# Performance work log

Hardware: AMD Instinct MI355X
Metric: run time of the kernel (lower is better)

## Reference

```python
import jax, jax.numpy as jnp
import numpy as np

NEG_INF = -9e15  # matches -9000000000000000.0 in torch code
ALPHA = 0.2      # LeakyReLU negative slope


def setup_inputs() -> dict:
    key = jax.random.key(0)
    k1, k2, k3, k4 = jax.random.split(key, 4)
    B, N, Fin, Fout = 8, 2048, 256, 256
    h = jax.random.normal(k1, (B, N, Fin), dtype=jnp.float32)
    adj = jax.random.randint(k2, (B, N, N), 0, 2, dtype=jnp.int32)
    W = jax.random.normal(k3, (Fin, Fout), dtype=jnp.float32) * 0.05
    a = jax.random.normal(k4, (2 * Fout, 1), dtype=jnp.float32) * 0.05
    return {"h": h, "adj": adj, "W": W, "a": a}


def reference(h, adj, W, a):
    # h: [B,N,Fin], adj: [B,N,N], W: [Fin,Fout], a: [2*Fout,1]
    Fout = W.shape[1]
    Wh = jnp.matmul(h, W)                       # [B,N,Fout]
    # Decompose concat-based additive score: e_ij = LReLU(a1.Wh_i + a2.Wh_j)
    a1 = a[:Fout, 0]                            # source-node part
    a2 = a[Fout:, 0]                            # target-node part
    s1 = jnp.einsum('bnf,f->bn', Wh, a1)        # [B,N]
    s2 = jnp.einsum('bnf,f->bn', Wh, a2)        # [B,N]
    e = jax.nn.leaky_relu(s1[:, :, None] + s2[:, None, :], negative_slope=ALPHA)  # [B,N,N]
    attn = jnp.where(adj > 0, e, NEG_INF)
    attn = jax.nn.softmax(attn, axis=2)          # masked softmax over neighbors
    # dropout omitted (deterministic eval-mode reference)
    h_prime = jnp.matmul(attn, Wh)               # [B,N,Fout]
    return h_prime
```

## Files before the change

### kernel.cpp

```cpp
#include <hip/hip_runtime.h>
#include <cstdint>

#define ALPHA 0.2f

constexpr int NB = 8;
constexpr int NN = 2048;
constexpr int NF = 256;

typedef __attribute__((ext_vector_type(8))) short bf16x8;
typedef __attribute__((ext_vector_type(4))) float f32x4;

__device__ __forceinline__ float bf2f(unsigned short u) {
    union { unsigned int i; float f; } v;
    v.i = ((unsigned int)u) << 16;
    return v.f;
}
__device__ __forceinline__ unsigned short f2bf(float f) {
    union { float f; unsigned int i; } v;
    v.f = f;
    v.i += 0x7fffu + ((v.i >> 16) & 1);
    return (unsigned short)(v.i >> 16);
}

__global__ __launch_bounds__(256) void k_wt(const float* __restrict__ W,
                                            unsigned short* __restrict__ WT,
                                            float* __restrict__ s1,
                                            float* __restrict__ s2) {
    const int t = threadIdx.x;
    const int gid = blockIdx.x * 256 + t;
    s1[gid] = 0.f;
    s2[gid] = 0.f;
    const int k = blockIdx.x * 4 + (t >> 6);
    const int f0 = (t & 63) * 4;
    const float4 w = *(const float4*)&W[k * NF + f0];
    WT[(f0 + 0) * NF + k] = f2bf(w.x);
    WT[(f0 + 1) * NF + k] = f2bf(w.y);
    WT[(f0 + 2) * NF + k] = f2bf(w.z);
    WT[(f0 + 3) * NF + k] = f2bf(w.w);
}

__global__ __launch_bounds__(256, 4) void k_wh(const float* __restrict__ h,
                                               const unsigned short* __restrict__ WT,
                                               const float* __restrict__ a,
                                               unsigned short* __restrict__ WhT,
                                               float* __restrict__ s1,
                                               float* __restrict__ s2) {
    __shared__ __align__(16) unsigned short As[64][72];
    __shared__ __align__(16) unsigned short Bs[64][72];
    const int tid = threadIdx.x;
    const int lane = tid & 63;
    const int l16 = lane & 15;
    const int quad = lane >> 4;
    const int wave = tid >> 6;
    const int row0 = (blockIdx.x >> 2) * 64;
    const int col0 = (blockIdx.x & 3) * 64;
    const int bb = row0 >> 11;
    const int n0 = row0 & (NN - 1);
    const int mb = (wave & 1) * 32;
    const int nb = (wave >> 1) * 32;

    f32x4 acc[2][2];
#pragma unroll
    for (int mf = 0; mf < 2; ++mf)
#pragma unroll
        for (int nf = 0; nf < 2; ++nf) acc[mf][nf] = (f32x4){0.f, 0.f, 0.f, 0.f};

    for (int k0 = 0; k0 < NF; k0 += 64) {
#pragma unroll
        for (int it = 0; it < 4; ++it) {
            const int q = tid + it * 256;
            const int r = q >> 4;
            const int k4 = (q & 15) * 4;
            const float4 v = *(const float4*)&h[(size_t)(row0 + r) * NF + k0 + k4];
            ushort4 o;
            o.x = f2bf(v.x); o.y = f2bf(v.y); o.z = f2bf(v.z); o.w = f2bf(v.w);
            *(ushort4*)&As[r][k4] = o;
        }
#pragma unroll
        for (int it = 0; it < 2; ++it) {
            const int q = tid + it * 256;
            const int f = q >> 3;
            const int k8 = (q & 7) * 8;
            *(uint4*)&Bs[f][k8] =
                *(const uint4*)&WT[(size_t)(col0 + f) * NF + k0 + k8];
        }
        __syncthreads();
#pragma unroll
        for (int ks = 0; ks < 64; ks += 32) {
            bf16x8 av[2], bv[2];
#pragma unroll
            for (int mf = 0; mf < 2; ++mf)
                av[mf] = *(const bf16x8*)&As[mb + mf * 16 + l16][ks + quad * 8];
#pragma unroll
            for (int nf = 0; nf < 2; ++nf)
                bv[nf] = *(const bf16x8*)&Bs[nb + nf * 16 + l16][ks + quad * 8];
#pragma unroll
            for (int mf = 0; mf < 2; ++mf)
#pragma unroll
                for (int nf = 0; nf < 2; ++nf)
                    acc[mf][nf] = __builtin_amdgcn_mfma_f32_16x16x32_bf16(
                        av[mf], bv[nf], acc[mf][nf], 0, 0, 0);
        }
        __syncthreads();
    }

#pragma unroll
    for (int mf = 0; mf < 2; ++mf) {
#pragma unroll
        for (int nf = 0; nf < 2; ++nf) {
            const size_t f = col0 + nb + nf * 16 + l16;
            const int nr = n0 + mb + mf * 16 + quad * 4;
            ushort4 o;
            o.x = f2bf(acc[mf][nf][0]);
            o.y = f2bf(acc[mf][nf][1]);
            o.z = f2bf(acc[mf][nf][2]);
            o.w = f2bf(acc[mf][nf][3]);
            *(ushort4*)&WhT[((size_t)bb * NF + f) * NN + nr] = o;
        }
    }

    float a1v[2], a2v[2];
#pragma unroll
    for (int nf = 0; nf < 2; ++nf) {
        const int f = col0 + nb + nf * 16 + l16;
        a1v[nf] = a[f];
        a2v[nf] = a[NF + f];
    }
#pragma unroll
    for (int mf = 0; mf < 2; ++mf) {
#pragma unroll
        for (int r = 0; r < 4; ++r) {
            float p1 = acc[mf][0][r] * a1v[0] + acc[mf][1][r] * a1v[1];
            float p2 = acc[mf][0][r] * a2v[0] + acc[mf][1][r] * a2v[1];
            p1 += __shfl_xor(p1, 1); p2 += __shfl_xor(p2, 1);
            p1 += __shfl_xor(p1, 2); p2 += __shfl_xor(p2, 2);
            p1 += __shfl_xor(p1, 4); p2 += __shfl_xor(p2, 4);
            p1 += __shfl_xor(p1, 8); p2 += __shfl_xor(p2, 8);
            if (l16 == 0) {
                const int n = n0 + mb + mf * 16 + quad * 4 + r;
                atomicAdd(&s1[bb * NN + n], p1);
                atomicAdd(&s2[bb * NN + n], p2);
            }
        }
    }
}

__global__ __launch_bounds__(256, 3) void k_attn(const unsigned short* __restrict__ WhT,
                                                 const int* __restrict__ adj,
                                                 const float* __restrict__ s1g,
                                                 const float* __restrict__ s2g,
                                                 float* __restrict__ out) {
    __shared__ __align__(16) unsigned short Pb[32][72];
    __shared__ float s1_s[32];
    __shared__ float l_s[32];

    const int tid = threadIdx.x;
    const int lane = tid & 63;
    const int l16 = lane & 15;
    const int quad = lane >> 4;
    const int wave = tid >> 6;
    const int bb = blockIdx.x >> 6;
    const int i0 = (blockIdx.x & 63) * 32;

    if (tid < 32) {
        s1_s[tid] = s1g[bb * NN + i0 + tid];
        l_s[tid] = 0.f;
    }
    __syncthreads();

    f32x4 acc[2][4];
#pragma unroll
    for (int m = 0; m < 2; ++m)
#pragma unroll
        for (int nf = 0; nf < 4; ++nf) acc[m][nf] = (f32x4){0.f, 0.f, 0.f, 0.f};

    const size_t whtBase = (size_t)bb * NF * NN;
    const size_t adjBase = (size_t)bb * NN * NN;
    const float* s2b = s2g + bb * NN;

    const int pIr = tid >> 4;
    const int pKq = (tid & 15) * 4;
    const int* adjP0 = &adj[adjBase + (size_t)(i0 + pIr) * NN + pKq];
    const int* adjP1 = adjP0 + 16 * NN;
    const float* s2P = &s2b[pKq];
    const unsigned short* whW = &WhT[whtBase + (size_t)(wave * 64 + l16) * NN + quad * 8];

    bf16x8 w0, w1, w2, w3, w4, w5, w6, w7;
    int4 amA0, amA1, amB0, amB1;
    float4 svA, svB;

#define B_LOAD(J0)                                                    \
    do {                                                              \
        const int j_ = (J0);                                          \
        w0 = *(const bf16x8*)&whW[(size_t)(0 * 16) * NN + j_ + 0];    \
        w1 = *(const bf16x8*)&whW[(size_t)(0 * 16) * NN + j_ + 32];   \
        w2 = *(const bf16x8*)&whW[(size_t)(1 * 16) * NN + j_ + 0];    \
        w3 = *(const bf16x8*)&whW[(size_t)(1 * 16) * NN + j_ + 32];   \
        w4 = *(const bf16x8*)&whW[(size_t)(2 * 16) * NN + j_ + 0];    \
        w5 = *(const bf16x8*)&whW[(size_t)(2 * 16) * NN + j_ + 32];   \
        w6 = *(const bf16x8*)&whW[(size_t)(3 * 16) * NN + j_ + 0];    \
        w7 = *(const bf16x8*)&whW[(size_t)(3 * 16) * NN + j_ + 32];   \
    } while (0)

#define ADJ_LOAD(AM0, AM1, SV, J0)                                    \
    do {                                                              \
        const int j_ = (J0);                                          \
        AM0 = *(const int4*)&adjP0[j_];                               \
        AM1 = *(const int4*)&adjP1[j_];                               \
        SV = *(const float4*)&s2P[j_];                                \
    } while (0)

#define P_HALF(AV, SV, IR)                                            \
    do {                                                              \
        const float s1v = s1_s[IR];                                   \
        float x0 = s1v + SV.x, x1 = s1v + SV.y;                       \
        float x2 = s1v + SV.z, x3 = s1v + SV.w;                       \
        x0 = x0 > 0.f ? x0 : ALPHA * x0;                              \
        x1 = x1 > 0.f ? x1 : ALPHA * x1;                              \
        x2 = x2 > 0.f ? x2 : ALPHA * x2;                              \
        x3 = x3 > 0.f ? x3 : ALPHA * x3;                              \
        const float p0 = AV.x > 0 ? __expf(x0) : 0.f;                 \
        const float p1 = AV.y > 0 ? __expf(x1) : 0.f;                 \
        const float p2 = AV.z > 0 ? __expf(x2) : 0.f;                 \
        const float p3 = AV.w > 0 ? __expf(x3) : 0.f;                 \
        uint2 pk;                                                     \
        pk.x = (unsigned int)f2bf(p0) | ((unsigned int)f2bf(p1) << 16);\
        pk.y = (unsigned int)f2bf(p2) | ((unsigned int)f2bf(p3) << 16);\
        *(uint2*)&Pb[IR][pKq] = pk;                                   \
        float ps = (p0 + p1) + (p2 + p3);                             \
        ps += __shfl_xor(ps, 8);                                      \
        ps += __shfl_xor(ps, 4);                                      \
        ps += __shfl_xor(ps, 2);                                      \
        ps += __shfl_xor(ps, 1);                                      \
        if ((tid & 15) == 0) l_s[IR] += ps;                           \
    } while (0)

#define MFMA_PHASE()                                                  \
    do {                                                              \
        bf16x8 af0 = *(const bf16x8*)&Pb[l16][quad * 8];              \
        bf16x8 af1 = *(const bf16x8*)&Pb[16 + l16][quad * 8];         \
        acc[0][0] = __builtin_amdgcn_mfma_f32_16x16x32_bf16(af0, w0, acc[0][0], 0, 0, 0); \
        acc[1][0] = __builtin_amdgcn_mfma_f32_16x16x32_bf16(af1, w0, acc[1][0], 0, 0, 0); \
        acc[0][1] = __builtin_amdgcn_mfma_f32_16x16x32_bf16(af0, w2, acc[0][1], 0, 0, 0); \
        acc[1][1] = __builtin_amdgcn_mfma_f32_16x16x32_bf16(af1, w2, acc[1][1], 0, 0, 0); \
        acc[0][2] = __builtin_amdgcn_mfma_f32_16x16x32_bf16(af0, w4, acc[0][2], 0, 0, 0); \
        acc[1][2] = __builtin_amdgcn_mfma_f32_16x16x32_bf16(af1, w4, acc[1][2], 0, 0, 0); \
        acc[0][3] = __builtin_amdgcn_mfma_f32_16x16x32_bf16(af0, w6, acc[0][3], 0, 0, 0); \
        acc[1][3] = __builtin_amdgcn_mfma_f32_16x16x32_bf16(af1, w6, acc[1][3], 0, 0, 0); \
        af0 = *(const bf16x8*)&Pb[l16][32 + quad * 8];                \
        af1 = *(const bf16x8*)&Pb[16 + l16][32 + quad * 8];           \
        acc[0][0] = __builtin_amdgcn_mfma_f32_16x16x32_bf16(af0, w1, acc[0][0], 0, 0, 0); \
        acc[1][0] = __builtin_amdgcn_mfma_f32_16x16x32_bf16(af1, w1, acc[1][0], 0, 0, 0); \
        acc[0][1] = __builtin_amdgcn_mfma_f32_16x16x32_bf16(af0, w3, acc[0][1], 0, 0, 0); \
        acc[1][1] = __builtin_amdgcn_mfma_f32_16x16x32_bf16(af1, w3, acc[1][1], 0, 0, 0); \
        acc[0][2] = __builtin_amdgcn_mfma_f32_16x16x32_bf16(af0, w5, acc[0][2], 0, 0, 0); \
        acc[1][2] = __builtin_amdgcn_mfma_f32_16x16x32_bf16(af1, w5, acc[1][2], 0, 0, 0); \
        acc[0][3] = __builtin_amdgcn_mfma_f32_16x16x32_bf16(af0, w7, acc[0][3], 0, 0, 0); \
        acc[1][3] = __builtin_amdgcn_mfma_f32_16x16x32_bf16(af1, w7, acc[1][3], 0, 0, 0); \
    } while (0)

    constexpr int NT = NN / 64;
    ADJ_LOAD(amA0, amA1, svA, 0);
    ADJ_LOAD(amB0, amB1, svB, 64);
    B_LOAD(0);

    for (int t = 0; t < NT; t += 2) {
        P_HALF(amA0, svA, pIr);
        P_HALF(amA1, svA, pIr + 16);
        __syncthreads();
        MFMA_PHASE();
        B_LOAD((t + 1) * 64);
        {
            const int j2 = (t + 2 < NT) ? (t + 2) * 64 : 0;
            ADJ_LOAD(amA0, amA1, svA, j2);
        }
        __syncthreads();
        P_HALF(amB0, svB, pIr);
        P_HALF(amB1, svB, pIr + 16);
        __syncthreads();
        MFMA_PHASE();
        {
            const int j1 = (t + 2 < NT) ? (t + 2) * 64 : 0;
            B_LOAD(j1);
        }
        {
            const int j3 = (t + 3 < NT) ? (t + 3) * 64 : 0;
            ADJ_LOAD(amB0, amB1, svB, j3);
        }
        __syncthreads();
    }
#undef B_LOAD
#undef ADJ_LOAD
#undef P_HALF
#undef MFMA_PHASE

    if (tid < 32) l_s[tid] = 1.0f / l_s[tid];
    __syncthreads();

    const int f0 = wave * 64;
#pragma unroll
    for (int m = 0; m < 2; ++m) {
#pragma unroll
        for (int r = 0; r < 4; ++r) {
            const int row = m * 16 + quad * 4 + r;
            const float inv = l_s[row];
#pragma unroll
            for (int nf = 0; nf < 4; ++nf) {
                out[((size_t)bb * NN + i0 + row) * NF + f0 + nf * 16 + l16] =
                    acc[m][nf][r] * inv;
            }
        }
    }
}

extern "C" void kernel_launch(void* const* d_in, const int* in_sizes, int n_in,
                              void* d_out, int out_size, void* d_ws, size_t ws_size,
                              hipStream_t stream) {
    const float* h = (const float*)d_in[0];
    const int* adj = (const int*)d_in[1];
    const float* W = (const float*)d_in[2];
    const float* a = (const float*)d_in[3];
    float* out = (float*)d_out;

    unsigned short* WhT = (unsigned short*)d_ws;
    float* s1 = (float*)((char*)d_ws + (size_t)NB * NN * NF * sizeof(unsigned short));
    float* s2 = s1 + (size_t)NB * NN;
    unsigned short* WT = (unsigned short*)(s2 + (size_t)NB * NN);

    k_wt<<<dim3(64), dim3(256), 0, stream>>>(W, WT, s1, s2);
    k_wh<<<dim3((NB * NN / 64) * (NF / 64)), dim3(256), 0, stream>>>(h, WT, a, WhT, s1, s2);
    k_attn<<<dim3(NB * (NN / 32)), dim3(256), 0, stream>>>(WhT, adj, s1, s2, out);
}
```

Baseline: 257.6 us.

## Double-buffer P tiles and WhT registers, defer row-sum reduction to epilogue

Result: no change. 254.0 us (-1.4%).

```diff
diff --git a/kernel.cpp b/kernel.cpp
--- a/kernel.cpp
+++ b/kernel.cpp
@@ -21,6 +21,8 @@
     v.i += 0x7fffu + ((v.i >> 16) & 1);
     return (unsigned short)(v.i >> 16);
 }
+
+#define WBAR() asm volatile("s_waitcnt lgkmcnt(0)\n\ts_barrier" ::: "memory")
 
 __global__ __launch_bounds__(256) void k_wt(const float* __restrict__ W,
                                             unsigned short* __restrict__ WT,
@@ -145,13 +147,13 @@
     }
 }
 
-__global__ __launch_bounds__(256, 3) void k_attn(const unsigned short* __restrict__ WhT,
+__global__ __launch_bounds__(256, 2) void k_attn(const unsigned short* __restrict__ WhT,
                                                  const int* __restrict__ adj,
                                                  const float* __restrict__ s1g,
                                                  const float* __restrict__ s2g,
                                                  float* __restrict__ out) {
-    __shared__ __align__(16) unsigned short Pb[32][72];
-    __shared__ float s1_s[32];
+    __shared__ __align__(16) unsigned short PbA[32][72];
+    __shared__ __align__(16) unsigned short PbB[32][72];
     __shared__ float l_s[32];
 
     const int tid = threadIdx.x;
@@ -162,12 +164,6 @@
     const int bb = blockIdx.x >> 6;
     const int i0 = (blockIdx.x & 63) * 32;
 
-    if (tid < 32) {
-        s1_s[tid] = s1g[bb * NN + i0 + tid];
-        l_s[tid] = 0.f;
-    }
-    __syncthreads();
-
     f32x4 acc[2][4];
 #pragma unroll
     for (int m = 0; m < 2; ++m)
@@ -185,115 +181,121 @@
     const float* s2P = &s2b[pKq];
     const unsigned short* whW = &WhT[whtBase + (size_t)(wave * 64 + l16) * NN + quad * 8];
 
-    bf16x8 w0, w1, w2, w3, w4, w5, w6, w7;
+    const float s1v0 = s1g[bb * NN + i0 + pIr];
+    const float s1v1 = s1g[bb * NN + i0 + 16 + pIr];
+    float lacc0 = 0.f, lacc1 = 0.f;
+
+    bf16x8 wa0, wa1, wa2, wa3, wa4, wa5, wa6, wa7;
+    bf16x8 wb0, wb1, wb2, wb3, wb4, wb5, wb6, wb7;
     int4 amA0, amA1, amB0, amB1;
     float4 svA, svB;
 
-#define B_LOAD(J0)                                                    \
-    do {                                                              \
-        const int j_ = (J0);                                          \
-        w0 = *(const bf16x8*)&whW[(size_t)(0 * 16) * NN + j_ + 0];    \
-        w1 = *(const bf16x8*)&whW[(size_t)(0 * 16) * NN + j_ + 32];   \
-        w2 = *(const bf16x8*)&whW[(size_t)(1 * 16) * NN + j_ + 0];    \
-        w3 = *(const bf16x8*)&whW[(size_t)(1 * 16) * NN + j_ + 32];   \
-        w4 = *(const bf16x8*)&whW[(size_t)(2 * 16) * NN + j_ + 0];    \
-        w5 = *(const bf16x8*)&whW[(size_t)(2 * 16) * NN + j_ + 32];   \
-        w6 = *(const bf16x8*)&whW[(size_t)(3 * 16) * NN + j_ + 0];    \
-        w7 = *(const bf16x8*)&whW[(size_t)(3 * 16) * NN + j_ + 32];   \
+#define B_LOAD(P, J0)                                                  \
+    do {                                                               \
+        const int j_ = (J0);                                           \
+        P##0 = *(const bf16x8*)&whW[(size_t)(0 * 16) * NN + j_ + 0];   \
+        P##1 = *(const bf16x8*)&whW[(size_t)(0 * 16) * NN + j_ + 32];  \
+        P##2 = *(const bf16x8*)&whW[(size_t)(1 * 16) * NN + j_ + 0];   \
+        P##3 = *(const bf16x8*)&whW[(size_t)(1 * 16) * NN + j_ + 32];  \
+        P##4 = *(const bf16x8*)&whW[(size_t)(2 * 16) * NN + j_ + 0];   \
+        P##5 = *(const bf16x8*)&whW[(size_t)(2 * 16) * NN + j_ + 32];  \
+        P##6 = *(const bf16x8*)&whW[(size_t)(3 * 16) * NN + j_ + 0];   \
+        P##7 = *(const bf16x8*)&whW[(size_t)(3 * 16) * NN + j_ + 32];  \
     } while (0)
 
-#define ADJ_LOAD(AM0, AM1, SV, J0)                                    \
-    do {                                                              \
-        const int j_ = (J0);                                          \
-        AM0 = *(const int4*)&adjP0[j_];                               \
-        AM1 = *(const int4*)&adjP1[j_];                               \
-        SV = *(const float4*)&s2P[j_];                                \
+#define ADJ_LOAD(AM0, AM1, SV, J0)                                     \
+    do {                                                               \
+        const int j_ = (J0);                                           \
+        AM0 = *(const int4*)&adjP0[j_];                                \
+        AM1 = *(const int4*)&adjP1[j_];                                \
+        SV = *(const float4*)&s2P[j_];                                 \
     } while (0)
 
-#define P_HALF(AV, SV, IR)                                            \
-    do {                                                              \
-        const float s1v = s1_s[IR];                                   \
-        float x0 = s1v + SV.x, x1 = s1v + SV.y;                       \
-        float x2 = s1v + SV.z, x3 = s1v + SV.w;                       \
-        x0 = x0 > 0.f ? x0 : ALPHA * x0;                              \
-        x1 = x1 > 0.f ? x1 : ALPHA * x1;                              \
-        x2 = x2 > 0.f ? x2 : ALPHA * x2;                              \
-        x3 = x3 > 0.f ? x3 : ALPHA * x3;                              \
-        const float p0 = AV.x > 0 ? __expf(x0) : 0.f;                 \
-        const float p1 = AV.y > 0 ? __expf(x1) : 0.f;                 \
-        const float p2 = AV.z > 0 ? __expf(x2) : 0.f;                 \
-        const float p3 = AV.w > 0 ? __expf(x3) : 0.f;                 \
-        uint2 pk;                                                     \
+#define P_HALF(AV, SV, S1V, IR, PB, LACC)                              \
+    do {                                                               \
+        float x0 = (S1V) + SV.x, x1 = (S1V) + SV.y;                    \
+        float x2 = (S1V) + SV.z, x3 = (S1V) + SV.w;                    \
+        x0 = x0 > 0.f ? x0 : ALPHA * x0;                               \
+        x1 = x1 > 0.f ? x1 : ALPHA * x1;                               \
+        x2 = x2 > 0.f ? x2 : ALPHA * x2;                               \
+        x3 = x3 > 0.f ? x3 : ALPHA * x3;                               \
+        const float p0 = AV.x > 0 ? __expf(x0) : 0.f;                  \
+        const float p1 = AV.y > 0 ? __expf(x1) : 0.f;                  \
+        const float p2 = AV.z > 0 ? __expf(x2) : 0.f;                  \
+        const float p3 = AV.w > 0 ? __expf(x3) : 0.f;                  \
+        uint2 pk;                                                      \
         pk.x = (unsigned int)f2bf(p0) | ((unsigned int)f2bf(p1) << 16);\
         pk.y = (unsigned int)f2bf(p2) | ((unsigned int)f2bf(p3) << 16);\
-        *(uint2*)&Pb[IR][pKq] = pk;                                   \
-        float ps = (p0 + p1) + (p2 + p3);                             \
-        ps += __shfl_xor(ps, 8);                                      \
-        ps += __shfl_xor(ps, 4);                                      \
-        ps += __shfl_xor(ps, 2);                                      \
-        ps += __shfl_xor(ps, 1);                                      \
-        if ((tid & 15) == 0) l_s[IR] += ps;                           \
+        *(uint2*)&PB[IR][pKq] = pk;                                    \
+        LACC += (p0 + p1) + (p2 + p3);                                 \
     } while (0)
 
-#define MFMA_PHASE()                                                  \
-    do {                                                              \
-        bf16x8 af0 = *(const bf16x8*)&Pb[l16][quad * 8];              \
-        bf16x8 af1 = *(const bf16x8*)&Pb[16 + l16][quad * 8];         \
-        acc[0][0] = __builtin_amdgcn_mfma_f32_16x16x32_bf16(af0, w0, acc[0][0], 0, 0, 0); \
-        acc[1][0] = __builtin_amdgcn_mfma_f32_16x16x32_bf16(af1, w0, acc[1][0], 0, 0, 0); \
-        acc[0][1] = __builtin_amdgcn_mfma_f32_16x16x32_bf16(af0, w2, acc[0][1], 0, 0, 0); \
-        acc[1][1] = __builtin_amdgcn_mfma_f32_16x16x32_bf16(af1, w2, acc[1][1], 0, 0, 0); \
-        acc[0][2] = __builtin_amdgcn_mfma_f32_16x16x32_bf16(af0, w4, acc[0][2], 0, 0, 0); \
-        acc[1][2] = __builtin_amdgcn_mfma_f32_16x16x32_bf16(af1, w4, acc[1][2], 0, 0, 0); \
-        acc[0][3] = __builtin_amdgcn_mfma_f32_16x16x32_bf16(af0, w6, acc[0][3], 0, 0, 0); \
-        acc[1][3] = __builtin_amdgcn_mfma_f32_16x16x32_bf16(af1, w6, acc[1][3], 0, 0, 0); \
-        af0 = *(const bf16x8*)&Pb[l16][32 + quad * 8];                \
-        af1 = *(const bf16x8*)&Pb[16 + l16][32 + quad * 8];           \
-        acc[0][0] = __builtin_amdgcn_mfma_f32_16x16x32_bf16(af0, w1, acc[0][0], 0, 0, 0); \
-        acc[1][0] = __builtin_amdgcn_mfma_f32_16x16x32_bf16(af1, w1, acc[1][0], 0, 0, 0); \
-        acc[0][1] = __builtin_amdgcn_mfma_f32_16x16x32_bf16(af0, w3, acc[0][1], 0, 0, 0); \
-        acc[1][1] = __builtin_amdgcn_mfma_f32_16x16x32_bf16(af1, w3, acc[1][1], 0, 0, 0); \
-        acc[0][2] = __builtin_amdgcn_mfma_f32_16x16x32_bf16(af0, w5, acc[0][2], 0, 0, 0); \
-        acc[1][2] = __builtin_amdgcn_mfma_f32_16x16x32_bf16(af1, w5, acc[1][2], 0, 0, 0); \
-        acc[0][3] = __builtin_amdgcn_mfma_f32_16x16x32_bf16(af0, w7, acc[0][3], 0, 0, 0); \
-        acc[1][3] = __builtin_amdgcn_mfma_f32_16x16x32_bf16(af1, w7, acc[1][3], 0, 0, 0); \
+#define MFMA_PHASE(PB, W)                                              \
+    do {                                                               \
+        bf16x8 af0 = *(const bf16x8*)&PB[l16][quad * 8];               \
+        bf16x8 af1 = *(const bf16x8*)&PB[16 + l16][quad * 8];          \
+        acc[0][0] = __builtin_amdgcn_mfma_f32_16x16x32_bf16(af0, W##0, acc[0][0], 0, 0, 0); \
+        acc[1][0] = __builtin_amdgcn_mfma_f32_16x16x32_bf16(af1, W##0, acc[1][0], 0, 0, 0); \
+        acc[0][1] = __builtin_amdgcn_mfma_f32_16x16x32_bf16(af0, W##2, acc[0][1], 0, 0, 0); \
+        acc[1][1] = __builtin_amdgcn_mfma_f32_16x16x32_bf16(af1, W##2, acc[1][1], 0, 0, 0); \
+        acc[0][2] = __builtin_amdgcn_mfma_f32_16x16x32_bf16(af0, W##4, acc[0][2], 0, 0, 0); \
+        acc[1][2] = __builtin_amdgcn_mfma_f32_16x16x32_bf16(af1, W##4, acc[1][2], 0, 0, 0); \
+        acc[0][3] = __builtin_amdgcn_mfma_f32_16x16x32_bf16(af0, W##6, acc[0][3], 0, 0, 0); \
+        acc[1][3] = __builtin_amdgcn_mfma_f32_16x16x32_bf16(af1, W##6, acc[1][3], 0, 0, 0); \
+        af0 = *(const bf16x8*)&PB[l16][32 + quad * 8];                 \
+        af1 = *(const bf16x8*)&PB[16 + l16][32 + quad * 8];            \
+        acc[0][0] = __builtin_amdgcn_mfma_f32_16x16x32_bf16(af0, W##1, acc[0][0], 0, 0, 0); \
+        acc[1][0] = __builtin_amdgcn_mfma_f32_16x16x32_bf16(af1, W##1, acc[1][0], 0, 0, 0); \
+        acc[0][1] = __builtin_amdgcn_mfma_f32_16x16x32_bf16(af0, W##3, acc[0][1], 0, 0, 0); \
+        acc[1][1] = __builtin_amdgcn_mfma_f32_16x16x32_bf16(af1, W##3, acc[1][1], 0, 0, 0); \
+        acc[0][2] = __builtin_amdgcn_mfma_f32_16x16x32_bf16(af0, W##5, acc[0][2], 0, 0, 0); \
+        acc[1][2] = __builtin_amdgcn_mfma_f32_16x16x32_bf16(af1, W##5, acc[1][2], 0, 0, 0); \
+        acc[0][3] = __builtin_amdgcn_mfma_f32_16x16x32_bf16(af0, W##7, acc[0][3], 0, 0, 0); \
+        acc[1][3] = __builtin_amdgcn_mfma_f32_16x16x32_bf16(af1, W##7, acc[1][3], 0, 0, 0); \
     } while (0)
 
     constexpr int NT = NN / 64;
     ADJ_LOAD(amA0, amA1, svA, 0);
     ADJ_LOAD(amB0, amB1, svB, 64);
-    B_LOAD(0);
+    B_LOAD(wa, 0);
 
     for (int t = 0; t < NT; t += 2) {
-        P_HALF(amA0, svA, pIr);
-        P_HALF(amA1, svA, pIr + 16);
-        __syncthreads();
-        MFMA_PHASE();
-        B_LOAD((t + 1) * 64);
+        B_LOAD(wb, (t + 1) * 64);
+        P_HALF(amA0, svA, s1v0, pIr, PbA, lacc0);
+        P_HALF(amA1, svA, s1v1, pIr + 16, PbA, lacc1);
         {
             const int j2 = (t + 2 < NT) ? (t + 2) * 64 : 0;
             ADJ_LOAD(amA0, amA1, svA, j2);
         }
-        __syncthreads();
-        P_HALF(amB0, svB, pIr);
-        P_HALF(amB1, svB, pIr + 16);
-        __syncthreads();
-        MFMA_PHASE();
+        WBAR();
+        MFMA_PHASE(PbA, wa);
         {
-            const int j1 = (t + 2 < NT) ? (t + 2) * 64 : 0;
-            B_LOAD(j1);
-        }
+            const int j2 = (t + 2 < NT) ? (t + 2) * 64 : 0;
+            B_LOAD(wa, j2);
+        }
+        P_HALF(amB0, svB, s1v0, pIr, PbB, lacc0);
+        P_HALF(amB1, svB, s1v1, pIr + 16, PbB, lacc1);
         {
             const int j3 = (t + 3 < NT) ? (t + 3) * 64 : 0;
             ADJ_LOAD(amB0, amB1, svB, j3);
         }
-        __syncthreads();
+        WBAR();
+        MFMA_PHASE(PbB, wb);
     }
 #undef B_LOAD
 #undef ADJ_LOAD
 #undef P_HALF
 #undef MFMA_PHASE
 
+    lacc0 += __shfl_xor(lacc0, 1); lacc1 += __shfl_xor(lacc1, 1);
+    lacc0 += __shfl_xor(lacc0, 2); lacc1 += __shfl_xor(lacc1, 2);
+    lacc0 += __shfl_xor(lacc0, 4); lacc1 += __shfl_xor(lacc1, 4);
+    lacc0 += __shfl_xor(lacc0, 8); lacc1 += __shfl_xor(lacc1, 8);
+    if ((tid & 15) == 0) {
+        l_s[pIr] = lacc0;
+        l_s[pIr + 16] = lacc1;
+    }
+    __syncthreads();
     if (tid < 32) l_s[tid] = 1.0f / l_s[tid];
     __syncthreads();
 
```
